# Kernel tuning notes

Hardware: AMD Instinct MI355X
Metric: run time of the kernel (lower is better)

Reference implementation:

```python
import jax, jax.numpy as jnp
import numpy as np

N = 8192      # total nodes (128 graphs x 64 electrodes)
L = 256       # signal_length
F = 64        # num_features
H = 128       # hidden_channels
G = 128       # num graphs
E = 262144    # num edges
C = 2         # n_classes


def setup_inputs() -> dict:
    key = jax.random.key(0)
    ks = jax.random.split(key, 20)
    def rn(k, shape, scale=0.05):
        return jax.random.normal(k, shape, jnp.float32) * scale
    return dict(
        x=jax.random.normal(ks[0], (N, L), jnp.float32),
        edge_index=jax.random.randint(ks[1], (2, E), 0, N),
        batch=jnp.repeat(jnp.arange(G), N // G),  # sorted graph id per node
        cw0=rn(ks[2], (F, 1, 7)), cb0=rn(ks[3], (F,)),
        cw_mid=rn(ks[4], (3, F, F, 5)), cb_mid=rn(ks[5], (3, F)),  # convs-2 = 3 middle convs
        cw_last=rn(ks[6], (F, F, 3)), cb_last=rn(ks[7], (F,)),
        enc_w=rn(ks[8], (F, F * 4)), enc_b=rn(ks[9], (F,)),  # in = F*((L-1)//2**6+1) = 256
        g0_rel_w=rn(ks[10], (H, F)), g0_rel_b=rn(ks[11], (H,)), g0_root_w=rn(ks[12], (H, F)),
        g_rel_w=rn(ks[13], (7, H, H)), g_rel_b=rn(ks[14], (7, H)), g_root_w=rn(ks[15], (7, H, H)),
        lin_w=rn(ks[16], (3, H, H)), lin_b=rn(ks[17], (3, H)),
        out_w=rn(ks[18], (C, H)), out_b=rn(ks[19], (C,)),
    )


def _conv1d(x, w, b, stride, pad):
    # x: [N, Cin, L], w: [Cout, Cin, K]
    y = jax.lax.conv_general_dilated(x, w, (stride,), [(pad, pad)],
                                     dimension_numbers=('NCH', 'OIH', 'NCH'))
    return y + b[None, :, None]


def reference(x, edge_index, batch, cw0, cb0, cw_mid, cb_mid, cw_last, cb_last,
              enc_w, enc_b, g0_rel_w, g0_rel_b, g0_root_w,
              g_rel_w, g_rel_b, g_root_w, lin_w, lin_b, out_w, out_b):
    act = jax.nn.relu
    rows = x.shape[0]
    h = x[:, None, :]                                    # [N, 1, L]
    h = act(_conv1d(h, cw0, cb0, 2, 3))                  # [N, F, L/2]
    for i in range(3):                                   # middle convs, k=5 s=2 p=2
        h = act(_conv1d(h, cw_mid[i], cb_mid[i], 2, 2))
    h = act(_conv1d(h, cw_last, cb_last, 2, 1))          # k=3 s=2 p=1 -> [N, F, 8]
    # AvgPool1d(k=3, s=2, p=1), count_include_pad=True -> always divide by 3
    h = jax.lax.reduce_window(h, 0.0, jax.lax.add, (1, 1, 3), (1, 1, 2),
                              [(0, 0), (0, 0), (1, 1)]) / 3.0   # [N, F, 4]
    h = h.reshape(rows, -1)                              # [N, F*4]
    h = h @ enc_w.T + enc_b                              # [N, F]
    src, dst = edge_index[0], edge_index[1]
    def gconv(h, rel_w, rel_b, root_w):
        # PyG GraphConv (aggr='add'): lin_rel(sum_j x_j) + lin_root(x)
        agg = jax.ops.segment_sum(h[src], dst, num_segments=N)
        return agg @ rel_w.T + rel_b + h @ root_w.T
    h = act(gconv(h, g0_rel_w, g0_rel_b, g0_root_w))     # hop 0: F -> H
    for i in range(7):                                   # hops 1..7: H -> H
        h = act(gconv(h, g_rel_w[i], g_rel_b[i], g_root_w[i]))
    # global mean pool by graph id
    sums = jax.ops.segment_sum(h, batch, num_segments=G)
    cnt = jax.ops.segment_sum(jnp.ones((N, 1), h.dtype), batch, num_segments=G)
    h = sums / jnp.maximum(cnt, 1.0)                     # [G, H]
    for i in range(3):
        h = act(h @ lin_w[i].T + lin_b[i])
    logits = h @ out_w.T + out_b                         # [G, C]
    return jax.nn.log_softmax(logits, -1)
```

## Files before the change

### kernel.cpp

```cpp
#include <hip/hip_runtime.h>
#include <hip/hip_bf16.h>

#define DEV_INLINE __device__ __forceinline__

typedef _Float16 f16;
typedef _Float16 f16x4 __attribute__((ext_vector_type(4)));
typedef _Float16 f16x8 __attribute__((ext_vector_type(8)));
typedef __bf16 bf16;
typedef __bf16 bf16x8 __attribute__((ext_vector_type(8)));
typedef float f32x16 __attribute__((ext_vector_type(16)));
typedef float f32x4 __attribute__((ext_vector_type(4)));

constexpr int N_NODES = 8192;
constexpr int G = 128;
constexpr int E_EDGES = 262144;


template<int MT, int LOG_PN, int IN_PS, int OUT_PS>
DEV_INLINE void conv_mid(const f16* __restrict__ wb, const float* __restrict__ bias,
                         char* inb, char* outb, int w, int l) {
  const int cht = w & 1;
  const int o_lane = cht * 32 + (l & 31);
  const int khalf = l >> 5;
  if ((w >> 1) < MT) {
    f16x8 wf[5][4];
#pragma unroll
    for (int k = 0; k < 5; k++)
#pragma unroll
      for (int s = 0; s < 4; s++)
        wf[k][s] = *(const f16x8*)&wb[(k * 64 + o_lane) * 64 + s * 16 + khalf * 8];
    f32x16 binit;
#pragma unroll
    for (int g = 0; g < 4; g++) {
      const float4 b4 = *(const float4*)&bias[cht * 32 + 8 * g + khalf * 4];
      binit[4 * g + 0] = b4.x; binit[4 * g + 1] = b4.y;
      binit[4 * g + 2] = b4.z; binit[4 * g + 3] = b4.w;
    }
    for (int mt = (w >> 1); mt < MT; mt += 2) {
      const int mo = mt * 32 + (l & 31);
      const int node = mo >> LOG_PN;
      const int po = mo & ((1 << LOG_PN) - 1);
      f32x16 acc = binit;
      f32x16 acc2 = {0,0,0,0,0,0,0,0,0,0,0,0,0,0,0,0};
#pragma unroll
      for (int k = 0; k < 5; k++) {
        const int d = k - 2;
        const int par = d & 1;
        const int row = po + (d >> 1) + 1;
        const char* rb = inb + ((node * 2 + par) * IN_PS + row) * 128;
        const int fx = row & 7;
#pragma unroll
        for (int s = 0; s < 4; s++) {
          const int c8 = 2 * s + khalf;
          f16x8 af = *(const f16x8*)(rb + ((c8 ^ fx) << 4));
          if (k & 1) acc2 = __builtin_amdgcn_mfma_f32_32x32x16_f16(wf[k][s], af, acc2, 0, 0, 0);
          else       acc  = __builtin_amdgcn_mfma_f32_32x32x16_f16(wf[k][s], af, acc, 0, 0, 0);
        }
      }
      const int orow = (po >> 1) + 1;
      const int ofx = orow & 7;
      char* base = outb + ((node * 2 + (po & 1)) * OUT_PS + orow) * 128 + khalf * 8;
#pragma unroll
      for (int g = 0; g < 4; g++) {
        f16x4 h4;
        h4[0] = (f16)fmaxf(acc[4 * g + 0] + acc2[4 * g + 0], 0.f);
        h4[1] = (f16)fmaxf(acc[4 * g + 1] + acc2[4 * g + 1], 0.f);
        h4[2] = (f16)fmaxf(acc[4 * g + 2] + acc2[4 * g + 2], 0.f);
        h4[3] = (f16)fmaxf(acc[4 * g + 3] + acc2[4 * g + 3], 0.f);
        *(f16x4*)(base + (((cht * 4 + g) ^ ofx) << 4)) = h4;
      }
    }
  }
}

struct alignas(16) L12LDS {
  union {
    char act1[2][2][66][128];
    char a2s[16384];
  } A;
  f16 xs16[2][272];
};

__global__ __launch_bounds__(256, 4) void conv_l1l2_kernel(
    const float* __restrict__ x,
    const f16* __restrict__ w0f, const float* __restrict__ cb0,
    const f16* __restrict__ wbmid, const float* __restrict__ cb_mid,
    f16* __restrict__ a2g) {
  __shared__ L12LDS lds;
  const int tid = threadIdx.x;
  const int w = tid >> 6, l = tid & 63;
  const int n0 = blockIdx.x * 2;

  for (int idx = tid; idx < 512; idx += 256) {
    int node = idx >> 8, j = idx & 255;
    lds.xs16[node][3 + j] = (f16)x[(size_t)(n0 + node) * 256 + j];
  }
  if (tid < 64) {
    int node = tid >> 5, t = tid & 31;
    int par = (t >> 3) & 1, hi = t >> 4, j = t & 7;
    *(int4*)&lds.A.act1[node][par][hi ? 65 : 0][j * 16] = make_int4(0, 0, 0, 0);
  } else if (tid < 96) {
    int t3 = tid - 64;
    int node = t3 >> 4, s = t3 & 15;
    int slot = (s < 3) ? s : (256 + s);
    lds.xs16[node][slot] = (f16)0.f;
  }
  __syncthreads();

  {
    const int cht = w & 1;
    const int o_lane = cht * 32 + (l & 31);
    const int khalf = l >> 5;
    const f16x8 w0frag = *(const f16x8*)&w0f[o_lane * 16 + khalf * 8];
    f32x16 binit;
#pragma unroll
    for (int g = 0; g < 4; g++) {
      const float4 b4 = *(const float4*)&cb0[cht * 32 + 8 * g + khalf * 4];
      binit[4 * g + 0] = b4.x; binit[4 * g + 1] = b4.y;
      binit[4 * g + 2] = b4.z; binit[4 * g + 3] = b4.w;
    }
    for (int mt = (w >> 1); mt < 8; mt += 2) {
      const int mo = mt * 32 + (l & 31);
      const int node = mo >> 7;
      const int po = mo & 127;
      union { uint u[4]; f16x8 v; } au;
      const char* ap = (const char*)&lds.xs16[node][2 * po + khalf * 8];
#pragma unroll
      for (int j = 0; j < 4; j++) au.u[j] = *(const uint*)(ap + 4 * j);
      f32x16 acc = __builtin_amdgcn_mfma_f32_32x32x16_f16(w0frag, au.v, binit, 0, 0, 0);
      const int orow = (po >> 1) + 1;
      const int ofx = orow & 7;
      char* base = (char*)lds.A.act1 + ((node * 2 + (po & 1)) * 66 + orow) * 128 + khalf * 8;
#pragma unroll
      for (int g = 0; g < 4; g++) {
        f16x4 h4;
        h4[0] = (f16)fmaxf(acc[4 * g + 0], 0.f);
        h4[1] = (f16)fmaxf(acc[4 * g + 1], 0.f);
        h4[2] = (f16)fmaxf(acc[4 * g + 2], 0.f);
        h4[3] = (f16)fmaxf(acc[4 * g + 3], 0.f);
        *(f16x4*)(base + (((cht * 4 + g) ^ ofx) << 4)) = h4;
      }
    }
  }
  __syncthreads();

  {
    const int cht = w & 1;
    const int o_lane = cht * 32 + (l & 31);
    const int khalf = l >> 5;
    f16x8 wf[5][4];
#pragma unroll
    for (int k = 0; k < 5; k++)
#pragma unroll
      for (int s = 0; s < 4; s++)
        wf[k][s] = *(const f16x8*)&wbmid[(k * 64 + o_lane) * 64 + s * 16 + khalf * 8];
    f32x16 binit;
#pragma unroll
    for (int g = 0; g < 4; g++) {
      const float4 b4 = *(const float4*)&cb_mid[cht * 32 + 8 * g + khalf * 4];
      binit[4 * g + 0] = b4.x; binit[4 * g + 1] = b4.y;
      binit[4 * g + 2] = b4.z; binit[4 * g + 3] = b4.w;
    }
    f16x4 outv[2][4];
#pragma unroll
    for (int it = 0; it < 2; it++) {
      const int mt = (w >> 1) + it * 2;
      const int mo = mt * 32 + (l & 31);
      const int node = mo >> 6;
      const int po = mo & 63;
      f32x16 acc = binit;
      f32x16 acc2 = {0,0,0,0,0,0,0,0,0,0,0,0,0,0,0,0};
#pragma unroll
      for (int k = 0; k < 5; k++) {
        const int d = k - 2;
        const int par = d & 1;
        const int row = po + (d >> 1) + 1;
        const char* rb = (char*)lds.A.act1 + ((node * 2 + par) * 66 + row) * 128;
        const int fx = row & 7;
#pragma unroll
        for (int s = 0; s < 4; s++) {
          const int c8 = 2 * s + khalf;
          f16x8 af = *(const f16x8*)(rb + ((c8 ^ fx) << 4));
          if (k & 1) acc2 = __builtin_amdgcn_mfma_f32_32x32x16_f16(wf[k][s], af, acc2, 0, 0, 0);
          else       acc  = __builtin_amdgcn_mfma_f32_32x32x16_f16(wf[k][s], af, acc, 0, 0, 0);
        }
      }
#pragma unroll
      for (int g = 0; g < 4; g++) {
        outv[it][g][0] = (f16)fmaxf(acc[4 * g + 0] + acc2[4 * g + 0], 0.f);
        outv[it][g][1] = (f16)fmaxf(acc[4 * g + 1] + acc2[4 * g + 1], 0.f);
        outv[it][g][2] = (f16)fmaxf(acc[4 * g + 2] + acc2[4 * g + 2], 0.f);
        outv[it][g][3] = (f16)fmaxf(acc[4 * g + 3] + acc2[4 * g + 3], 0.f);
      }
    }
    __syncthreads();
#pragma unroll
    for (int it = 0; it < 2; it++) {
      const int mt = (w >> 1) + it * 2;
      const int row = mt * 32 + (l & 31);
      char* base = lds.A.a2s + row * 128 + khalf * 8;
#pragma unroll
      for (int g = 0; g < 4; g++)
        *(f16x4*)(base + (((cht * 4 + g) ^ (row & 7)) << 4)) = outv[it][g];
    }
    __syncthreads();
    char* gout = (char*)a2g + (size_t)n0 * 8192;
#pragma unroll
    for (int i = 0; i < 4; i++) {
      const int idx = tid + i * 256;
      const int row = idx >> 3, s = idx & 7;
      int4 v = *(const int4*)(lds.A.a2s + row * 128 + ((s ^ (row & 7)) << 4));
      *(int4*)(gout + idx * 16) = v;
    }
  }
}

struct alignas(16) L3LDS {
  union {
    char in2[2][2][34][128];
    struct {
      float act5[16][68];
      float pooled[2][256];
      float encred[2][2][64];
    } t;
  } U;
  char act3[2][2][18][128];
  char act4[2][2][10][128];
};

__global__ __launch_bounds__(256, 4) void conv_l3tail_kernel(
    const f16* __restrict__ a2g,
    const f16* __restrict__ wbmid, const float* __restrict__ cb_mid,
    const f16* __restrict__ wb5, const float* __restrict__ cb_last,
    const f16* __restrict__ enc_w16, const float* __restrict__ enc_b,
    float* __restrict__ henc) {
  __shared__ L3LDS lds;
  const int tid = threadIdx.x;
  const int w = tid >> 6, l = tid & 63;
  const int n0 = blockIdx.x * 2;

#pragma unroll
  for (int i = 0; i < 4; i++) {
    const int idx = tid + i * 256;
    const int node = idx >> 9;
    const int rem = idx & 511;
    const int p = rem >> 3, s8 = rem & 7;
    const int row = (p >> 1) + 1, par = p & 1;
    int4 v = *(const int4*)&a2g[((size_t)(n0 + node) * 64 + p) * 64 + s8 * 8];
    *(int4*)((char*)lds.U.in2 + ((node * 2 + par) * 34 + row) * 128
             + ((s8 ^ (row & 7)) << 4)) = v;
  }
  if (tid < 192) {
    int which = tid >> 6;
    int t = tid & 63;
    int node = t >> 5, tt = t & 31;
    int par = (tt >> 3) & 1, hi = tt >> 4, j = tt & 7;
    if (which == 0)
      *(int4*)&lds.U.in2[node][par][hi ? 33 : 0][j * 16] = make_int4(0, 0, 0, 0);
    else if (which == 1)
      *(int4*)&lds.act3[node][par][hi ? 17 : 0][j * 16] = make_int4(0, 0, 0, 0);
    else
      *(int4*)&lds.act4[node][par][hi ? 9 : 0][j * 16] = make_int4(0, 0, 0, 0);
  }
  __syncthreads();

  conv_mid<2, 5, 34, 18>(wbmid + 5 * 64 * 64, cb_mid + 64,
                         (char*)lds.U.in2, (char*)lds.act3, w, l);
  __syncthreads();
  conv_mid<1, 4, 18, 10>(wbmid + 2 * 5 * 64 * 64, cb_mid + 128,
                         (char*)lds.act3, (char*)lds.act4, w, l);
  __syncthreads();

  {
    const int ch_row = w * 16 + (l & 15);
    const int kq = l >> 4;
    f16x8 wf5[3][2];
#pragma unroll
    for (int k = 0; k < 3; k++)
#pragma unroll
      for (int s = 0; s < 2; s++)
        wf5[k][s] = *(const f16x8*)&wb5[(k * 64 + ch_row) * 64 + s * 32 + kq * 8];
    const float4 b4 = *(const float4*)&cb_last[w * 16 + kq * 4];
    f32x4 acc5 = {b4.x, b4.y, b4.z, b4.w};
    const int m5 = l & 15, nd5 = m5 >> 3, p5 = m5 & 7;
#pragma unroll
    for (int k = 0; k < 3; k++) {
      const int d = k - 1;
      const int par = d & 1;
      const int row = p5 + (d >> 1) + 1;
      const char* rb = (char*)lds.act4 + ((nd5 * 2 + par) * 10 + row) * 128;
      const int fx = row & 7;
#pragma unroll
      for (int s = 0; s < 2; s++) {
        const int c8 = 4 * s + kq;
        f16x8 af = *(const f16x8*)(rb + ((c8 ^ fx) << 4));
        acc5 = __builtin_amdgcn_mfma_f32_16x16x32_f16(wf5[k][s], af, acc5, 0, 0, 0);
      }
    }
    f32x4 o4;
    o4[0] = fmaxf(acc5[0], 0.f);
    o4[1] = fmaxf(acc5[1], 0.f);
    o4[2] = fmaxf(acc5[2], 0.f);
    o4[3] = fmaxf(acc5[3], 0.f);
    *(f32x4*)&lds.U.t.act5[nd5 * 8 + p5][w * 16 + kq * 4] = o4;
  }
  __syncthreads();

  for (int jj = tid; jj < 512; jj += 256) {
    int node = jj >> 8, j = jj & 255;
    int c = j >> 2, q = j & 3;
    const float* a5 = &lds.U.t.act5[node * 8][0];
    float v = a5[(2 * q) * 68 + c] + a5[(2 * q + 1) * 68 + c];
    if (q > 0) v += a5[(2 * q - 1) * 68 + c];
    lds.U.t.pooled[node][j] = v * (1.f / 3.f);
  }
  __syncthreads();

  {
    const int node = tid >> 7, tt = tid & 127;
    const int o = tt & 63, jg = tt >> 6;
    float acc = 0.f;
    const f16x8* ew = (const f16x8*)&enc_w16[o * 256 + jg * 128];
    const float4* pj = (const float4*)&lds.U.t.pooled[node][jg * 128];
#pragma unroll 4
    for (int j8 = 0; j8 < 16; j8++) {
      f16x8 e8 = ew[j8];
      float4 p0 = pj[2 * j8], p1 = pj[2 * j8 + 1];
      acc += (float)e8[0] * p0.x + (float)e8[1] * p0.y +
             (float)e8[2] * p0.z + (float)e8[3] * p0.w +
             (float)e8[4] * p1.x + (float)e8[5] * p1.y +
             (float)e8[6] * p1.z + (float)e8[7] * p1.w;
    }
    lds.U.t.encred[node][jg][o] = acc;
  }
  __syncthreads();
  if (tid < 128) {
    int node = tid >> 6, o = tid & 63;
    henc[(size_t)(n0 + node) * 64 + o] =
        lds.U.t.encred[node][0][o] + lds.U.t.encred[node][1][o] + enc_b[o];
  }
}

__global__ void wprep_all(const float* __restrict__ cw0,
                          const float* __restrict__ cw_mid, const float* __restrict__ cw_last,
                          const float* __restrict__ enc_w,
                          const float* __restrict__ g0_rel, const float* __restrict__ g0_root,
                          const float* __restrict__ g0_rel_b,
                          const float* __restrict__ g_rel, const float* __restrict__ g_root,
                          const float* __restrict__ g_rel_b,
                          f16* __restrict__ w0f, f16* __restrict__ wbmid, f16* __restrict__ wb5,
                          f16* __restrict__ enc_w16,
                          bf16* __restrict__ wg, float* __restrict__ bg) {
  int idx = blockIdx.x * 256 + threadIdx.x;
  if (idx < 64 * 16) {
    int o = idx >> 4, k = idx & 15;
    w0f[idx] = (k < 7) ? (f16)cw0[o * 7 + k] : (f16)0.f;
  }
  if (idx < 3 * 5 * 64 * 64) {
    int lay = idx / (5 * 64 * 64);
    int rem = idx % (5 * 64 * 64);
    int k = rem / 4096;
    int o = (rem >> 6) & 63;
    int c = rem & 63;
    wbmid[idx] = (f16)cw_mid[((lay * 64 + o) * 64 + c) * 5 + k];
  } else {
    int i2 = idx - 3 * 5 * 64 * 64;
    if (i2 < 3 * 64 * 64) {
      int k = i2 / 4096;
      int o = (i2 >> 6) & 63;
      int c = i2 & 63;
      wb5[i2] = (f16)cw_last[(o * 64 + c) * 3 + k];
    }
  }
  if (idx < 64 * 256) enc_w16[idx] = (f16)enc_w[idx];
  if (idx < 128 * 128) {
    int o = idx >> 7, k = idx & 127;
    float v = (k < 64) ? g0_rel[o * 64 + k] : g0_root[o * 64 + (k - 64)];
    bf16 h = (bf16)v;
    wg[idx] = h;
    wg[128 * 128 + idx] = (bf16)(v - (float)h);
  }
  if (idx < 7 * 128 * 256) {
    int lsel = idx / (128 * 256);
    int r = idx % (128 * 256);
    int o = r >> 8, k = r & 255;
    float v = (k < 128) ? g_rel[(lsel * 128 + o) * 128 + k]
                        : g_root[(lsel * 128 + o) * 128 + (k - 128)];
    bf16 h = (bf16)v;
    size_t base = 2 * 128 * 128 + (size_t)lsel * 2 * 128 * 256;
    wg[base + r] = h;
    wg[base + 128 * 256 + r] = (bf16)(v - (float)h);
  }
  if (idx < 8 * 128) {
    int lsel = idx >> 7, o = idx & 127;
    bg[idx] = (lsel == 0) ? g0_rel_b[o] : g_rel_b[(lsel - 1) * 128 + o];
  }
}

__global__ void hist_kernel(const int* __restrict__ dst, int* __restrict__ cnt) {
  int e = blockIdx.x * 256 + threadIdx.x;
  atomicAdd(&cnt[dst[e]], 1);
}

__global__ void scan_kernel(const int* __restrict__ cnt, int* __restrict__ rp) {
  __shared__ int part[256];
  int t = threadIdx.x;
  int base = t * 32;
  int local[32];
  int s = 0;
#pragma unroll
  for (int i = 0; i < 32; i++) { local[i] = cnt[base + i]; s += local[i]; }
  part[t] = s;
  __syncthreads();
  for (int off = 1; off < 256; off <<= 1) {
    int v = (t >= off) ? part[t - off] : 0;
    __syncthreads();
    part[t] += v;
    __syncthreads();
  }
  int run = part[t] - s;
#pragma unroll
  for (int i = 0; i < 32; i++) { rp[base + i] = run; run += local[i]; }
  if (t == 255) rp[N_NODES] = run;
}

__global__ void fill_kernel(const int* __restrict__ src, const int* __restrict__ dst,
                            const int* __restrict__ rp, int* __restrict__ cur,
                            int* __restrict__ csr) {
  int e = blockIdx.x * 256 + threadIdx.x;
  int r = dst[e];
  int p = atomicAdd(&cur[r], 1);
  csr[rp[r] + p] = src[e];
}

template<int D>
__global__ __launch_bounds__(256) void gatherf(
    const float* __restrict__ h, const int* __restrict__ csr,
    const int* __restrict__ rp, float* __restrict__ agg) {
  constexpr int LPN = D / 4;
  const int node = blockIdx.x * (256 / LPN) + (threadIdx.x / LPN);
  const int cl = threadIdx.x & (LPN - 1);
  const int s = rp[node], e = rp[node + 1];
  float4 a0 = make_float4(0.f, 0.f, 0.f, 0.f);
  float4 a1 = make_float4(0.f, 0.f, 0.f, 0.f);
  float4 a2 = make_float4(0.f, 0.f, 0.f, 0.f);
  float4 a3 = make_float4(0.f, 0.f, 0.f, 0.f);
  int i = s;
  for (; i + 3 < e; i += 4) {
    const int m0 = csr[i], m1 = csr[i + 1], m2 = csr[i + 2], m3 = csr[i + 3];
    float4 v0 = *(const float4*)&h[(size_t)m0 * D + cl * 4];
    float4 v1 = *(const float4*)&h[(size_t)m1 * D + cl * 4];
    float4 v2 = *(const float4*)&h[(size_t)m2 * D + cl * 4];
    float4 v3 = *(const float4*)&h[(size_t)m3 * D + cl * 4];
    a0.x += v0.x; a0.y += v0.y; a0.z += v0.z; a0.w += v0.w;
    a1.x += v1.x; a1.y += v1.y; a1.z += v1.z; a1.w += v1.w;
    a2.x += v2.x; a2.y += v2.y; a2.z += v2.z; a2.w += v2.w;
    a3.x += v3.x; a3.y += v3.y; a3.z += v3.z; a3.w += v3.w;
  }
  for (; i < e; i++) {
    const int m0 = csr[i];
    float4 v0 = *(const float4*)&h[(size_t)m0 * D + cl * 4];
    a0.x += v0.x; a0.y += v0.y; a0.z += v0.z; a0.w += v0.w;
  }
  a0.x += a1.x + a2.x + a3.x;
  a0.y += a1.y + a2.y + a3.y;
  a0.z += a1.z + a2.z + a3.z;
  a0.w += a1.w + a2.w + a3.w;
  *(float4*)&agg[(size_t)node * D + cl * 4] = a0;
}

template<int K>
__global__ __launch_bounds__(256) void gnn_gemm_bf(
    const float* __restrict__ agg, const float* __restrict__ hroot,
    const bf16* __restrict__ wg, const float* __restrict__ bg,
    float* __restrict__ hout) {
  constexpr int F = K / 2;
  constexpr int ROWB = K * 2;
  constexpr int KSTEPS = K / 16;
  __shared__ alignas(16) char smem[2][32 * K * 2];
  const int tid = threadIdx.x;
  const int l = tid & 63, w = tid >> 6;
  const int n0 = blockIdx.x * 32;

  {
    const int row = tid >> 3, p = tid & 7;
    constexpr int cpp = K / 64;
#pragma unroll
    for (int j = 0; j < cpp; j++) {
      const int slot = p * cpp + j;
      const int c0 = slot * 8;
      const float* src = (c0 < F) ? &agg[(size_t)(n0 + row) * F + c0]
                                  : &hroot[(size_t)(n0 + row) * F + (c0 - F)];
      float4 v0 = ((const float4*)src)[0];
      float4 v1 = ((const float4*)src)[1];
      float vv[8] = {v0.x, v0.y, v0.z, v0.w, v1.x, v1.y, v1.z, v1.w};
      bf16x8 hi8, lo8;
#pragma unroll
      for (int e = 0; e < 8; e++) {
        float v = vv[e];
        bf16 h = (bf16)v;
        hi8[e] = h;
        lo8[e] = (bf16)(v - (float)h);
      }
      const int off = row * ROWB + ((slot ^ (row & 7)) << 4);
      *(bf16x8*)(smem[0] + off) = hi8;
      *(bf16x8*)(smem[1] + off) = lo8;
    }
  }

  const int ch = w * 32 + (l & 31);
  const int khalf = l >> 5;
  bf16x8 whi[KSTEPS], wlo[KSTEPS];
  const bf16* wrow = wg + (size_t)ch * K + khalf * 8;
#pragma unroll
  for (int ks = 0; ks < KSTEPS; ks++) {
    whi[ks] = *(const bf16x8*)&wrow[ks * 16];
    wlo[ks] = *(const bf16x8*)&wrow[128 * K + ks * 16];
  }
  const float bv = bg[ch];

  __syncthreads();

  const int row0 = l & 31;
  f32x16 acc = {0,0,0,0,0,0,0,0,0,0,0,0,0,0,0,0};
#pragma unroll
  for (int ks = 0; ks < KSTEPS; ks++) {
    const int slot = ks * 2 + khalf;
    const int off = row0 * ROWB + ((slot ^ (row0 & 7)) << 4);
    bf16x8 ah = *(const bf16x8*)(smem[0] + off);
    bf16x8 al = *(const bf16x8*)(smem[1] + off);
    acc = __builtin_amdgcn_mfma_f32_32x32x16_bf16(ah, whi[ks], acc, 0, 0, 0);
    acc = __builtin_amdgcn_mfma_f32_32x32x16_bf16(al, whi[ks], acc, 0, 0, 0);
    acc = __builtin_amdgcn_mfma_f32_32x32x16_bf16(ah, wlo[ks], acc, 0, 0, 0);
  }

#pragma unroll
  for (int r = 0; r < 16; r++) {
    const int nl = (r & 3) + 8 * (r >> 2) + 4 * khalf;
    hout[(size_t)(n0 + nl) * 128 + ch] = fmaxf(acc[r] + bv, 0.f);
  }
}

__global__ __launch_bounds__(256) void poolg(const float* __restrict__ h,
                                             float* __restrict__ pooled) {
  const int g = blockIdx.x;
  const int tid = threadIdx.x;
  const int ch = tid & 127, half = tid >> 7;
  const float* base = h + ((size_t)g * 64 + half * 32) * 128 + ch;
  float s = 0.f;
#pragma unroll 8
  for (int i = 0; i < 32; i++) s += base[(size_t)i * 128];
  __shared__ float red[256];
  red[tid] = s;
  __syncthreads();
  if (tid < 128) pooled[(size_t)g * 128 + tid] = (red[tid] + red[tid + 128]) * (1.f / 64.f);
}

__global__ __launch_bounds__(128) void mlp_kernel(
    const float* __restrict__ pooled,
    const float* __restrict__ lin_w, const float* __restrict__ lin_b,
    const float* __restrict__ out_w, const float* __restrict__ out_b,
    float* __restrict__ out) {
  const int g = blockIdx.x;
  const int t = threadIdx.x;
  __shared__ float hs[128];
  __shared__ float lg[2];
  hs[t] = pooled[(size_t)g * 128 + t];
  __syncthreads();
  for (int lsel = 0; lsel < 3; lsel++) {
    float acc = lin_b[lsel * 128 + t];
    for (int j = 0; j < 128; j++) acc += hs[j] * lin_w[(lsel * 128 + t) * 128 + j];
    __syncthreads();
    hs[t] = fmaxf(acc, 0.f);
    __syncthreads();
  }
  if (t < 2) {
    float acc = out_b[t];
    for (int j = 0; j < 128; j++) acc += hs[j] * out_w[t * 128 + j];
    lg[t] = acc;
  }
  __syncthreads();
  if (t < 2) {
    float m = fmaxf(lg[0], lg[1]);
    float lse = m + logf(expf(lg[0] - m) + expf(lg[1] - m));
    out[g * 2 + t] = lg[t] - lse;
  }
}

extern "C" void kernel_launch(void* const* d_in, const int* in_sizes, int n_in,
                              void* d_out, int out_size, void* d_ws, size_t ws_size,
                              hipStream_t stream) {
  const float* x       = (const float*)d_in[0];
  const int*   edge    = (const int*)d_in[1];
  const float* cw0     = (const float*)d_in[3];
  const float* cb0     = (const float*)d_in[4];
  const float* cw_mid  = (const float*)d_in[5];
  const float* cb_mid  = (const float*)d_in[6];
  const float* cw_last = (const float*)d_in[7];
  const float* cb_last = (const float*)d_in[8];
  const float* enc_w   = (const float*)d_in[9];
  const float* enc_b   = (const float*)d_in[10];
  const float* g0_rel_w  = (const float*)d_in[11];
  const float* g0_rel_b  = (const float*)d_in[12];
  const float* g0_root_w = (const float*)d_in[13];
  const float* g_rel_w   = (const float*)d_in[14];
  const float* g_rel_b   = (const float*)d_in[15];
  const float* g_root_w  = (const float*)d_in[16];
  const float* lin_w     = (const float*)d_in[17];
  const float* lin_b     = (const float*)d_in[18];
  const float* out_w     = (const float*)d_in[19];
  const float* out_b     = (const float*)d_in[20];
  float* out = (float*)d_out;

  const int* esrc = edge;
  const int* edst = edge + E_EDGES;

  char* ws = (char*)d_ws;
  size_t off = 0;
  auto alloc = [&](size_t bytes) {
    void* p = ws + off;
    off += (bytes + 255) & ~size_t(255);
    return p;
  };
  float* henc = (float*)alloc((size_t)N_NODES * 64 * 4);
  float* hA   = (float*)alloc((size_t)N_NODES * 128 * 4);
  float* hB   = (float*)alloc((size_t)N_NODES * 128 * 4);
  float* agg  = (float*)alloc((size_t)N_NODES * 128 * 4);
  bf16* wg    = (bf16*)alloc((size_t)(128 * 128 + 7 * 128 * 256) * 2 * 2);
  float* bg   = (float*)alloc((size_t)8 * 128 * 4);
  float* pooled = (float*)alloc((size_t)G * 128 * 4);
  int* cnt  = (int*)alloc((size_t)N_NODES * 4);
  int* rp   = (int*)alloc((size_t)(N_NODES + 1) * 4);
  int* cur  = (int*)alloc((size_t)N_NODES * 4);
  int* csr  = (int*)alloc((size_t)E_EDGES * 4);
  f16* w0f   = (f16*)alloc((size_t)64 * 16 * 2);
  f16* wbmid = (f16*)alloc((size_t)3 * 5 * 64 * 64 * 2);
  f16* wb5   = (f16*)alloc((size_t)3 * 64 * 64 * 2);
  f16* enc_w16 = (f16*)alloc((size_t)64 * 256 * 2);
  f16* a2g   = (f16*)alloc((size_t)N_NODES * 64 * 64 * 2);

  hipMemsetAsync(cnt, 0, (size_t)N_NODES * 4, stream);
  hipMemsetAsync(cur, 0, (size_t)N_NODES * 4, stream);

  wprep_all<<<896, 256, 0, stream>>>(cw0, cw_mid, cw_last, enc_w,
                                     g0_rel_w, g0_root_w, g0_rel_b,
                                     g_rel_w, g_root_w, g_rel_b,
                                     w0f, wbmid, wb5, enc_w16, wg, bg);
  conv_l1l2_kernel<<<N_NODES / 2, 256, 0, stream>>>(x, w0f, cb0, wbmid, cb_mid, a2g);
  conv_l3tail_kernel<<<N_NODES / 2, 256, 0, stream>>>(
      a2g, wbmid, cb_mid, wb5, cb_last, enc_w16, enc_b, henc);

  hist_kernel<<<E_EDGES / 256, 256, 0, stream>>>(edst, cnt);
  scan_kernel<<<1, 256, 0, stream>>>(cnt, rp);
  fill_kernel<<<E_EDGES / 256, 256, 0, stream>>>(esrc, edst, rp, cur, csr);

  gatherf<64><<<N_NODES / 16, 256, 0, stream>>>(henc, csr, rp, agg);
  gnn_gemm_bf<128><<<N_NODES / 32, 256, 0, stream>>>(agg, henc, wg, bg, hA);

  float* hprev = hA;
  float* hnext = hB;
  for (int lsel = 0; lsel < 7; lsel++) {
    gatherf<128><<<N_NODES / 8, 256, 0, stream>>>(hprev, csr, rp, agg);
    gnn_gemm_bf<256><<<N_NODES / 32, 256, 0, stream>>>(
        agg, hprev, wg + 2 * 128 * 128 + (size_t)lsel * 2 * 128 * 256,
        bg + (lsel + 1) * 128, hnext);
    float* tmp = hprev; hprev = hnext; hnext = tmp;
  }

  poolg<<<G, 256, 0, stream>>>(hprev, pooled);
  mlp_kernel<<<G, 128, 0, stream>>>(pooled, lin_w, lin_b, out_w, out_b, out);
}
```

Before: 371.1 us.

## Fuse neighbor gather into GraphConv GEMM kernel and drop split accumulator

Merges the separate CSR gather kernel into the bf16 split-precision GEMM kernel, so each block sums its 32 nodes' neighbor features directly into shared memory instead of round-tripping through a global agg buffer. This removes one launch per hop and the agg write and read traffic. In exchange, each block has only 256 threads gathering with 8 lanes per node, which may lower memory-level parallelism for the irregular gather compared with the dedicated kernel. It also folds the two alternating MFMA accumulators in the conv layer into one, which lengthens the MFMA dependency chain.

```diff
diff --git a/kernel.cpp b/kernel.cpp
--- a/kernel.cpp
+++ b/kernel.cpp
@@ -14,7 +14,6 @@
 constexpr int N_NODES = 8192;
 constexpr int G = 128;
 constexpr int E_EDGES = 262144;
-
 
 template<int MT, int LOG_PN, int IN_PS, int OUT_PS>
 DEV_INLINE void conv_mid(const f16* __restrict__ wb, const float* __restrict__ bias,
@@ -169,7 +168,6 @@
       const int node = mo >> 6;
       const int po = mo & 63;
       f32x16 acc = binit;
-      f32x16 acc2 = {0,0,0,0,0,0,0,0,0,0,0,0,0,0,0,0};
 #pragma unroll
       for (int k = 0; k < 5; k++) {
         const int d = k - 2;
@@ -181,16 +179,15 @@
         for (int s = 0; s < 4; s++) {
           const int c8 = 2 * s + khalf;
           f16x8 af = *(const f16x8*)(rb + ((c8 ^ fx) << 4));
-          if (k & 1) acc2 = __builtin_amdgcn_mfma_f32_32x32x16_f16(wf[k][s], af, acc2, 0, 0, 0);
-          else       acc  = __builtin_amdgcn_mfma_f32_32x32x16_f16(wf[k][s], af, acc, 0, 0, 0);
+          acc = __builtin_amdgcn_mfma_f32_32x32x16_f16(wf[k][s], af, acc, 0, 0, 0);
         }
       }
 #pragma unroll
       for (int g = 0; g < 4; g++) {
-        outv[it][g][0] = (f16)fmaxf(acc[4 * g + 0] + acc2[4 * g + 0], 0.f);
-        outv[it][g][1] = (f16)fmaxf(acc[4 * g + 1] + acc2[4 * g + 1], 0.f);
-        outv[it][g][2] = (f16)fmaxf(acc[4 * g + 2] + acc2[4 * g + 2], 0.f);
-        outv[it][g][3] = (f16)fmaxf(acc[4 * g + 3] + acc2[4 * g + 3], 0.f);
+        outv[it][g][0] = (f16)fmaxf(acc[4 * g + 0], 0.f);
+        outv[it][g][1] = (f16)fmaxf(acc[4 * g + 1], 0.f);
+        outv[it][g][2] = (f16)fmaxf(acc[4 * g + 2], 0.f);
+        outv[it][g][3] = (f16)fmaxf(acc[4 * g + 3], 0.f);
       }
     }
     __syncthreads();
@@ -433,81 +430,21 @@
   csr[rp[r] + p] = src[e];
 }
 
-template<int D>
-__global__ __launch_bounds__(256) void gatherf(
+template<int K>
+__global__ __launch_bounds__(256) void gnn_fused(
     const float* __restrict__ h, const int* __restrict__ csr,
-    const int* __restrict__ rp, float* __restrict__ agg) {
-  constexpr int LPN = D / 4;
-  const int node = blockIdx.x * (256 / LPN) + (threadIdx.x / LPN);
-  const int cl = threadIdx.x & (LPN - 1);
-  const int s = rp[node], e = rp[node + 1];
-  float4 a0 = make_float4(0.f, 0.f, 0.f, 0.f);
-  float4 a1 = make_float4(0.f, 0.f, 0.f, 0.f);
-  float4 a2 = make_float4(0.f, 0.f, 0.f, 0.f);
-  float4 a3 = make_float4(0.f, 0.f, 0.f, 0.f);
-  int i = s;
-  for (; i + 3 < e; i += 4) {
-    const int m0 = csr[i], m1 = csr[i + 1], m2 = csr[i + 2], m3 = csr[i + 3];
-    float4 v0 = *(const float4*)&h[(size_t)m0 * D + cl * 4];
-    float4 v1 = *(const float4*)&h[(size_t)m1 * D + cl * 4];
-    float4 v2 = *(const float4*)&h[(size_t)m2 * D + cl * 4];
-    float4 v3 = *(const float4*)&h[(size_t)m3 * D + cl * 4];
-    a0.x += v0.x; a0.y += v0.y; a0.z += v0.z; a0.w += v0.w;
-    a1.x += v1.x; a1.y += v1.y; a1.z += v1.z; a1.w += v1.w;
-    a2.x += v2.x; a2.y += v2.y; a2.z += v2.z; a2.w += v2.w;
-    a3.x += v3.x; a3.y += v3.y; a3.z += v3.z; a3.w += v3.w;
-  }
-  for (; i < e; i++) {
-    const int m0 = csr[i];
-    float4 v0 = *(const float4*)&h[(size_t)m0 * D + cl * 4];
-    a0.x += v0.x; a0.y += v0.y; a0.z += v0.z; a0.w += v0.w;
-  }
-  a0.x += a1.x + a2.x + a3.x;
-  a0.y += a1.y + a2.y + a3.y;
-  a0.z += a1.z + a2.z + a3.z;
-  a0.w += a1.w + a2.w + a3.w;
-  *(float4*)&agg[(size_t)node * D + cl * 4] = a0;
-}
-
-template<int K>
-__global__ __launch_bounds__(256) void gnn_gemm_bf(
-    const float* __restrict__ agg, const float* __restrict__ hroot,
+    const int* __restrict__ rp,
     const bf16* __restrict__ wg, const float* __restrict__ bg,
     float* __restrict__ hout) {
   constexpr int F = K / 2;
   constexpr int ROWB = K * 2;
   constexpr int KSTEPS = K / 16;
+  constexpr int NV = F / 32;
   __shared__ alignas(16) char smem[2][32 * K * 2];
   const int tid = threadIdx.x;
   const int l = tid & 63, w = tid >> 6;
   const int n0 = blockIdx.x * 32;
 
-  {
-    const int row = tid >> 3, p = tid & 7;
-    constexpr int cpp = K / 64;
-#pragma unroll
-    for (int j = 0; j < cpp; j++) {
-      const int slot = p * cpp + j;
-      const int c0 = slot * 8;
-      const float* src = (c0 < F) ? &agg[(size_t)(n0 + row) * F + c0]
-                                  : &hroot[(size_t)(n0 + row) * F + (c0 - F)];
-      float4 v0 = ((const float4*)src)[0];
-      float4 v1 = ((const float4*)src)[1];
-      float vv[8] = {v0.x, v0.y, v0.z, v0.w, v1.x, v1.y, v1.z, v1.w};
-      bf16x8 hi8, lo8;
-#pragma unroll
-      for (int e = 0; e < 8; e++) {
-        float v = vv[e];
-        bf16 h = (bf16)v;
-        hi8[e] = h;
-        lo8[e] = (bf16)(v - (float)h);
-      }
-      const int off = row * ROWB + ((slot ^ (row & 7)) << 4);
-      *(bf16x8*)(smem[0] + off) = hi8;
-      *(bf16x8*)(smem[1] + off) = lo8;
-    }
-  }
-
   const int ch = w * 32 + (l & 31);
   const int khalf = l >> 5;
   bf16x8 whi[KSTEPS], wlo[KSTEPS];
@@ -519,6 +456,86 @@
   }
   const float bv = bg[ch];
 
+  {
+    const int row = tid >> 3, p = tid & 7;
+    const int node = n0 + row;
+    const int c0 = p * (F / 8);
+    const int s = rp[node], e = rp[node + 1];
+    float4 av[NV], av2[NV];
+#pragma unroll
+    for (int v = 0; v < NV; v++) {
+      av[v] = make_float4(0.f, 0.f, 0.f, 0.f);
+      av2[v] = make_float4(0.f, 0.f, 0.f, 0.f);
+    }
+    int i = s;
+    for (; i + 1 < e; i += 2) {
+      const int m0 = csr[i], m1 = csr[i + 1];
+      const float4* p0 = (const float4*)&h[(size_t)m0 * F + c0];
+      const float4* p1 = (const float4*)&h[(size_t)m1 * F + c0];
+#pragma unroll
+      for (int v = 0; v < NV; v++) {
+        float4 q0 = p0[v], q1 = p1[v];
+        av[v].x += q0.x; av[v].y += q0.y; av[v].z += q0.z; av[v].w += q0.w;
+        av2[v].x += q1.x; av2[v].y += q1.y; av2[v].z += q1.z; av2[v].w += q1.w;
+      }
+    }
+    if (i < e) {
+      const int m0 = csr[i];
+      const float4* p0 = (const float4*)&h[(size_t)m0 * F + c0];
+#pragma unroll
+      for (int v = 0; v < NV; v++) {
+        float4 q0 = p0[v];
+        av[v].x += q0.x; av[v].y += q0.y; av[v].z += q0.z; av[v].w += q0.w;
+      }
+    }
+    float gv[NV * 4];
+#pragma unroll
+    for (int v = 0; v < NV; v++) {
+      gv[4 * v + 0] = av[v].x + av2[v].x;
+      gv[4 * v + 1] = av[v].y + av2[v].y;
+      gv[4 * v + 2] = av[v].z + av2[v].z;
+      gv[4 * v + 3] = av[v].w + av2[v].w;
+    }
+    const int swz = row & 7;
+#pragma unroll
+    for (int g = 0; g < NV / 2; g++) {
+      bf16x8 hi8, lo8;
+#pragma unroll
+      for (int e2 = 0; e2 < 8; e2++) {
+        float v = gv[g * 8 + e2];
+        bf16 hh = (bf16)v;
+        hi8[e2] = hh;
+        lo8[e2] = (bf16)(v - (float)hh);
+      }
+      const int slot = p * (NV / 2) + g;
+      const int off = row * ROWB + ((slot ^ swz) << 4);
+      *(bf16x8*)(smem[0] + off) = hi8;
+      *(bf16x8*)(smem[1] + off) = lo8;
+    }
+    const float4* hr = (const float4*)&h[(size_t)node * F + c0];
+    float rv[NV * 4];
+#pragma unroll
+    for (int v = 0; v < NV; v++) {
+      float4 q = hr[v];
+      rv[4 * v + 0] = q.x; rv[4 * v + 1] = q.y;
+      rv[4 * v + 2] = q.z; rv[4 * v + 3] = q.w;
+    }
+#pragma unroll
+    for (int g = 0; g < NV / 2; g++) {
+      bf16x8 hi8, lo8;
+#pragma unroll
+      for (int e2 = 0; e2 < 8; e2++) {
+        float v = rv[g * 8 + e2];
+        bf16 hh = (bf16)v;
+        hi8[e2] = hh;
+        lo8[e2] = (bf16)(v - (float)hh);
+      }
+      const int slot = F / 8 + p * (NV / 2) + g;
+      const int off = row * ROWB + ((slot ^ swz) << 4);
+      *(bf16x8*)(smem[0] + off) = hi8;
+      *(bf16x8*)(smem[1] + off) = lo8;
+    }
+  }
   __syncthreads();
 
   const int row0 = l & 31;
@@ -625,7 +642,6 @@
   float* henc = (float*)alloc((size_t)N_NODES * 64 * 4);
   float* hA   = (float*)alloc((size_t)N_NODES * 128 * 4);
   float* hB   = (float*)alloc((size_t)N_NODES * 128 * 4);
-  float* agg  = (float*)alloc((size_t)N_NODES * 128 * 4);
   bf16* wg    = (bf16*)alloc((size_t)(128 * 128 + 7 * 128 * 256) * 2 * 2);
   float* bg   = (float*)alloc((size_t)8 * 128 * 4);
   float* pooled = (float*)alloc((size_t)G * 128 * 4);
@@ -654,15 +670,13 @@
   scan_kernel<<<1, 256, 0, stream>>>(cnt, rp);
   fill_kernel<<<E_EDGES / 256, 256, 0, stream>>>(esrc, edst, rp, cur, csr);
 
-  gatherf<64><<<N_NODES / 16, 256, 0, stream>>>(henc, csr, rp, agg);
-  gnn_gemm_bf<128><<<N_NODES / 32, 256, 0, stream>>>(agg, henc, wg, bg, hA);
+  gnn_fused<128><<<N_NODES / 32, 256, 0, stream>>>(henc, csr, rp, wg, bg, hA);
 
   float* hprev = hA;
   float* hnext = hB;
   for (int lsel = 0; lsel < 7; lsel++) {
-    gatherf<128><<<N_NODES / 8, 256, 0, stream>>>(hprev, csr, rp, agg);
-    gnn_gemm_bf<256><<<N_NODES / 32, 256, 0, stream>>>(
-        agg, hprev, wg + 2 * 128 * 128 + (size_t)lsel * 2 * 128 * 256,
+    gnn_fused<256><<<N_NODES / 32, 256, 0, stream>>>(
+        hprev, csr, rp, wg + 2 * 128 * 128 + (size_t)lsel * 2 * 128 * 256,
         bg + (lsel + 1) * 128, hnext);
     float* tmp = hprev; hprev = hnext; hnext = tmp;
   }
```

Measured after the change: 400.2 us. 7.8% more time.

## Process four nodes per block in conv layer-3 tail kernel; merge split accumulators

Applied to the files above, without the earlier changes.

The conv_l3tail kernel now handles four nodes per block instead of two. This halves the grid and spreads each block's per-wave weight-fragment loads over twice as many MFMA tiles. LDS buffers double and launch bounds drop from 4 to 2 blocks per CU, which may reduce occupancy. Separately, the l1l2 conv loop drops its second accumulator and chains all MFMAs into one accumulator. That lowers register use but lengthens the MFMA dependency chain.

```diff
diff --git a/kernel.cpp b/kernel.cpp
--- a/kernel.cpp
+++ b/kernel.cpp
@@ -14,7 +14,6 @@
 constexpr int N_NODES = 8192;
 constexpr int G = 128;
 constexpr int E_EDGES = 262144;
-
 
 template<int MT, int LOG_PN, int IN_PS, int OUT_PS>
 DEV_INLINE void conv_mid(const f16* __restrict__ wb, const float* __restrict__ bias,
@@ -169,7 +168,6 @@
       const int node = mo >> 6;
       const int po = mo & 63;
       f32x16 acc = binit;
-      f32x16 acc2 = {0,0,0,0,0,0,0,0,0,0,0,0,0,0,0,0};
 #pragma unroll
       for (int k = 0; k < 5; k++) {
         const int d = k - 2;
@@ -181,16 +179,15 @@
         for (int s = 0; s < 4; s++) {
           const int c8 = 2 * s + khalf;
           f16x8 af = *(const f16x8*)(rb + ((c8 ^ fx) << 4));
-          if (k & 1) acc2 = __builtin_amdgcn_mfma_f32_32x32x16_f16(wf[k][s], af, acc2, 0, 0, 0);
-          else       acc  = __builtin_amdgcn_mfma_f32_32x32x16_f16(wf[k][s], af, acc, 0, 0, 0);
+          acc = __builtin_amdgcn_mfma_f32_32x32x16_f16(wf[k][s], af, acc, 0, 0, 0);
         }
       }
 #pragma unroll
       for (int g = 0; g < 4; g++) {
-        outv[it][g][0] = (f16)fmaxf(acc[4 * g + 0] + acc2[4 * g + 0], 0.f);
-        outv[it][g][1] = (f16)fmaxf(acc[4 * g + 1] + acc2[4 * g + 1], 0.f);
-        outv[it][g][2] = (f16)fmaxf(acc[4 * g + 2] + acc2[4 * g + 2], 0.f);
-        outv[it][g][3] = (f16)fmaxf(acc[4 * g + 3] + acc2[4 * g + 3], 0.f);
+        outv[it][g][0] = (f16)fmaxf(acc[4 * g + 0], 0.f);
+        outv[it][g][1] = (f16)fmaxf(acc[4 * g + 1], 0.f);
+        outv[it][g][2] = (f16)fmaxf(acc[4 * g + 2], 0.f);
+        outv[it][g][3] = (f16)fmaxf(acc[4 * g + 3], 0.f);
       }
     }
     __syncthreads();
@@ -217,18 +214,18 @@
 
 struct alignas(16) L3LDS {
   union {
-    char in2[2][2][34][128];
+    char in2[4][2][34][128];
     struct {
-      float act5[16][68];
-      float pooled[2][256];
-      float encred[2][2][64];
+      float act5[32][68];
+      float pooled[4][256];
+      float encred[4][2][64];
     } t;
   } U;
-  char act3[2][2][18][128];
-  char act4[2][2][10][128];
+  char act3[4][2][18][128];
+  char act4[4][2][10][128];
 };
 
-__global__ __launch_bounds__(256, 4) void conv_l3tail_kernel(
+__global__ __launch_bounds__(256, 2) void conv_l3tail_kernel(
     const f16* __restrict__ a2g,
     const f16* __restrict__ wbmid, const float* __restrict__ cb_mid,
     const f16* __restrict__ wb5, const float* __restrict__ cb_last,
@@ -237,10 +234,10 @@
   __shared__ L3LDS lds;
   const int tid = threadIdx.x;
   const int w = tid >> 6, l = tid & 63;
-  const int n0 = blockIdx.x * 2;
-
-#pragma unroll
-  for (int i = 0; i < 4; i++) {
+  const int n0 = blockIdx.x * 4;
+
+#pragma unroll
+  for (int i = 0; i < 8; i++) {
     const int idx = tid + i * 256;
     const int node = idx >> 9;
     const int rem = idx & 511;
@@ -250,9 +247,9 @@
     *(int4*)((char*)lds.U.in2 + ((node * 2 + par) * 34 + row) * 128
              + ((s8 ^ (row & 7)) << 4)) = v;
   }
-  if (tid < 192) {
-    int which = tid >> 6;
-    int t = tid & 63;
+  for (int gg = tid; gg < 384; gg += 256) {
+    int which = gg >> 7;
+    int t = gg & 127;
     int node = t >> 5, tt = t & 31;
     int par = (tt >> 3) & 1, hi = tt >> 4, j = tt & 7;
     if (which == 0)
@@ -264,10 +261,10 @@
   }
   __syncthreads();
 
-  conv_mid<2, 5, 34, 18>(wbmid + 5 * 64 * 64, cb_mid + 64,
+  conv_mid<4, 5, 34, 18>(wbmid + 5 * 64 * 64, cb_mid + 64,
                          (char*)lds.U.in2, (char*)lds.act3, w, l);
   __syncthreads();
-  conv_mid<1, 4, 18, 10>(wbmid + 2 * 5 * 64 * 64, cb_mid + 128,
+  conv_mid<2, 4, 18, 10>(wbmid + 2 * 5 * 64 * 64, cb_mid + 128,
                          (char*)lds.act3, (char*)lds.act4, w, l);
   __syncthreads();
 
@@ -281,32 +278,36 @@
       for (int s = 0; s < 2; s++)
         wf5[k][s] = *(const f16x8*)&wb5[(k * 64 + ch_row) * 64 + s * 32 + kq * 8];
     const float4 b4 = *(const float4*)&cb_last[w * 16 + kq * 4];
-    f32x4 acc5 = {b4.x, b4.y, b4.z, b4.w};
-    const int m5 = l & 15, nd5 = m5 >> 3, p5 = m5 & 7;
-#pragma unroll
-    for (int k = 0; k < 3; k++) {
-      const int d = k - 1;
-      const int par = d & 1;
-      const int row = p5 + (d >> 1) + 1;
-      const char* rb = (char*)lds.act4 + ((nd5 * 2 + par) * 10 + row) * 128;
-      const int fx = row & 7;
-#pragma unroll
-      for (int s = 0; s < 2; s++) {
-        const int c8 = 4 * s + kq;
-        f16x8 af = *(const f16x8*)(rb + ((c8 ^ fx) << 4));
-        acc5 = __builtin_amdgcn_mfma_f32_16x16x32_f16(wf5[k][s], af, acc5, 0, 0, 0);
+#pragma unroll
+    for (int pt = 0; pt < 2; pt++) {
+      f32x4 acc5 = {b4.x, b4.y, b4.z, b4.w};
+      const int pos = pt * 16 + (l & 15);
+      const int nd5 = pos >> 3, p5 = pos & 7;
+#pragma unroll
+      for (int k = 0; k < 3; k++) {
+        const int d = k - 1;
+        const int par = d & 1;
+        const int row = p5 + (d >> 1) + 1;
+        const char* rb = (char*)lds.act4 + ((nd5 * 2 + par) * 10 + row) * 128;
+        const int fx = row & 7;
+#pragma unroll
+        for (int s = 0; s < 2; s++) {
+          const int c8 = 4 * s + kq;
+          f16x8 af = *(const f16x8*)(rb + ((c8 ^ fx) << 4));
+          acc5 = __builtin_amdgcn_mfma_f32_16x16x32_f16(wf5[k][s], af, acc5, 0, 0, 0);
+        }
       }
-    }
-    f32x4 o4;
-    o4[0] = fmaxf(acc5[0], 0.f);
-    o4[1] = fmaxf(acc5[1], 0.f);
-    o4[2] = fmaxf(acc5[2], 0.f);
-    o4[3] = fmaxf(acc5[3], 0.f);
-    *(f32x4*)&lds.U.t.act5[nd5 * 8 + p5][w * 16 + kq * 4] = o4;
-  }
-  __syncthreads();
-
-  for (int jj = tid; jj < 512; jj += 256) {
+      f32x4 o4;
+      o4[0] = fmaxf(acc5[0], 0.f);
+      o4[1] = fmaxf(acc5[1], 0.f);
+      o4[2] = fmaxf(acc5[2], 0.f);
+      o4[3] = fmaxf(acc5[3], 0.f);
+      *(f32x4*)&lds.U.t.act5[pos][w * 16 + kq * 4] = o4;
+    }
+  }
+  __syncthreads();
+
+  for (int jj = tid; jj < 1024; jj += 256) {
     int node = jj >> 8, j = jj & 255;
     int c = j >> 2, q = j & 3;
     const float* a5 = &lds.U.t.act5[node * 8][0];
@@ -316,8 +317,9 @@
   }
   __syncthreads();
 
-  {
-    const int node = tid >> 7, tt = tid & 127;
+  for (int nn = 0; nn < 4; nn += 2) {
+    const int node = nn + (tid >> 7);
+    const int tt = tid & 127;
     const int o = tt & 63, jg = tt >> 6;
     float acc = 0.f;
     const f16x8* ew = (const f16x8*)&enc_w16[o * 256 + jg * 128];
@@ -334,7 +336,7 @@
     lds.U.t.encred[node][jg][o] = acc;
   }
   __syncthreads();
-  if (tid < 128) {
+  {
     int node = tid >> 6, o = tid & 63;
     henc[(size_t)(n0 + node) * 64 + o] =
         lds.U.t.encred[node][0][o] + lds.U.t.encred[node][1][o] + enc_b[o];
@@ -647,7 +649,7 @@
                                      g_rel_w, g_root_w, g_rel_b,
                                      w0f, wbmid, wb5, enc_w16, wg, bg);
   conv_l1l2_kernel<<<N_NODES / 2, 256, 0, stream>>>(x, w0f, cb0, wbmid, cb_mid, a2g);
-  conv_l3tail_kernel<<<N_NODES / 2, 256, 0, stream>>>(
+  conv_l3tail_kernel<<<N_NODES / 4, 256, 0, stream>>>(
       a2g, wbmid, cb_mid, wb5, cb_last, enc_w16, enc_b, henc);
 
   hist_kernel<<<E_EDGES / 256, 256, 0, stream>>>(edst, cnt);
```

Result: faster. 352.0 us (-5.2%).
